# Kernel tuning notes

Hardware: AMD Instinct MI355X
Metric: run time of the kernel (lower is better)

## Reference

```python
import jax, jax.numpy as jnp
import numpy as np


def setup_inputs() -> dict:
    key = jax.random.key(0)
    k1, k2 = jax.random.split(key)
    B, S, D = 32, 1024, 384
    MAX_MEL_LEN = 8192  # >= max possible sum of durations (7*1024)
    x = jax.random.normal(k1, (B, S, D), dtype=jnp.float32)
    duration = jax.random.randint(k2, (B, S), 0, 8, dtype=jnp.int32)
    return {"x": x, "duration": duration, "max_mel_len": MAX_MEL_LEN}


def reference(x, duration, max_mel_len):
    # x: (B, S, D) float, duration: (B, S) int, max_mel_len: python int
    B, S, D = x.shape
    csum = jnp.cumsum(duration, axis=1)          # (B, S) inclusive cumsum
    mel_len = csum[:, -1]                        # (B,) expanded length per sample
    t = jnp.arange(max_mel_len, dtype=csum.dtype)  # (T,) output frame indices
    # frame t maps to token i where csum[i-1] <= t < csum[i]; side='right'
    # correctly skips zero-duration tokens (repeated csum values)
    idx = jax.vmap(lambda c: jnp.searchsorted(c, t, side='right'))(csum)  # (B, T)
    idx = jnp.clip(idx, 0, S - 1)
    out = jnp.take_along_axis(x, idx[:, :, None], axis=1)  # (B, T, D) gather
    mask = t[None, :] < mel_len[:, None]                   # (B, T) pad mask
    out = out * mask[:, :, None].astype(x.dtype)
    return out, mel_len.astype(jnp.int64)
```

## Files before the change

kernel.cpp:

```cpp
#include <hip/hip_runtime.h>


#define BATCH 32
#define SRC_S 1024
#define DIM   384
#define ROWS  32
#define C4    (DIM / 4)

typedef float f32x4 __attribute__((ext_vector_type(4)));

__global__ void lr_scan_idx_kernel(const int* __restrict__ duration,
                                   int* __restrict__ idx_g,
                                   float* __restrict__ mel_out, int T) {
    __shared__ int s[SRC_S];
    const int b = blockIdx.x;
    const int tid = threadIdx.x;
    const int d = duration[b * SRC_S + tid];
    s[tid] = d;
    for (int off = 1; off < SRC_S; off <<= 1) {
        __syncthreads();
        const int add = (tid >= off) ? s[tid - off] : 0;
        __syncthreads();
        s[tid] += add;
    }
    __syncthreads();
    const int end = s[tid];
    const int start = end - d;
    const int mel_len = s[SRC_S - 1];

    int* __restrict__ ib = idx_g + (size_t)b * T;
    for (int t = start; t < end; ++t) ib[t] = tid;
    for (int t = mel_len + tid; t < T; t += SRC_S) ib[t] = -1;

    if (tid == SRC_S - 1) mel_out[b] = (float)mel_len;
}

__global__ __launch_bounds__(256)
void lr_gather_kernel(const f32x4* __restrict__ x4,
                      const int* __restrict__ idx_g,
                      f32x4* __restrict__ out4, int T) {
    const int b = blockIdx.y;
    const int t0 = blockIdx.x * ROWS;
    const int tid = threadIdx.x;

    const int* __restrict__ ib = idx_g + (size_t)b * T + t0;
    const f32x4* __restrict__ xb = x4 + (size_t)b * SRC_S * C4;
    f32x4* __restrict__ ob = out4 + ((size_t)b * T + t0) * C4;

    #pragma unroll
    for (int k = 0; k < (ROWS * C4) / 256; ++k) {
        const int i = tid + k * 256;
        const int row = i / C4;
        const int col = i - row * C4;
        const int sidx = ib[row];
        f32x4 v = (f32x4)(0.f);
        if (sidx >= 0) v = xb[(size_t)sidx * C4 + col];
        __builtin_nontemporal_store(v, &ob[i]);
    }
}

extern "C" void kernel_launch(void* const* d_in, const int* in_sizes, int n_in,
                              void* d_out, int out_size, void* d_ws, size_t ws_size,
                              hipStream_t stream) {
    const float* x = (const float*)d_in[0];
    const int* duration = (const int*)d_in[1];
    const int T = (out_size - BATCH) / (BATCH * DIM);

    int* idx_g = (int*)d_ws;
    float* out = (float*)d_out;
    float* mel_out = out + (size_t)BATCH * T * DIM;

    lr_scan_idx_kernel<<<BATCH, SRC_S, 0, stream>>>(duration, idx_g, mel_out, T);

    dim3 grid((T + ROWS - 1) / ROWS, BATCH);
    lr_gather_kernel<<<grid, 256, 0, stream>>>((const f32x4*)x, idx_g,
                                               (f32x4*)out, T);
}
```

Before: 446.3 us.

## Use wavefront shuffle scan and XCD-aware block mapping for gather

Replaces the shared-memory Hillis-Steele scan with a two-level wavefront shuffle scan, cutting the number of block barriers. The gather grid is flattened and remapped so that all blocks of a given batch land on the same XCD, keeping that batch's source rows in one L2 slice. The mapping hardcodes 256 tiles per batch (T/ROWS) and 8 XCDs, so it only holds for T=8192 and assumes round-robin dispatch across XCDs.

```diff
diff --git a/kernel.cpp b/kernel.cpp
--- a/kernel.cpp
+++ b/kernel.cpp
@@ -6,27 +6,42 @@
 #define DIM   384
 #define ROWS  32
 #define C4    (DIM / 4)
+#define NXCD  8
 
 typedef float f32x4 __attribute__((ext_vector_type(4)));
 
 __global__ void lr_scan_idx_kernel(const int* __restrict__ duration,
                                    int* __restrict__ idx_g,
                                    float* __restrict__ mel_out, int T) {
-    __shared__ int s[SRC_S];
+    __shared__ int wsum[16];
     const int b = blockIdx.x;
     const int tid = threadIdx.x;
+    const int lane = tid & 63;
+    const int wid = tid >> 6;
     const int d = duration[b * SRC_S + tid];
-    s[tid] = d;
-    for (int off = 1; off < SRC_S; off <<= 1) {
-        __syncthreads();
-        const int add = (tid >= off) ? s[tid - off] : 0;
-        __syncthreads();
-        s[tid] += add;
+
+    int v = d;
+    #pragma unroll
+    for (int off = 1; off < 64; off <<= 1) {
+        const int n = __shfl_up(v, off, 64);
+        if (lane >= off) v += n;
+    }
+    if (lane == 63) wsum[wid] = v;
+    __syncthreads();
+    if (tid < 16) {
+        int w = wsum[tid];
+        #pragma unroll
+        for (int off = 1; off < 16; off <<= 1) {
+            const int n = __shfl_up(w, off, 64);
+            if (tid >= off) w += n;
+        }
+        wsum[tid] = w;
     }
     __syncthreads();
-    const int end = s[tid];
+    const int wbase = (wid == 0) ? 0 : wsum[wid - 1];
+    const int end = wbase + v;
     const int start = end - d;
-    const int mel_len = s[SRC_S - 1];
+    const int mel_len = wsum[15];
 
     int* __restrict__ ib = idx_g + (size_t)b * T;
     for (int t = start; t < end; ++t) ib[t] = tid;
@@ -39,8 +54,11 @@
 void lr_gather_kernel(const f32x4* __restrict__ x4,
                       const int* __restrict__ idx_g,
                       f32x4* __restrict__ out4, int T) {
-    const int b = blockIdx.y;
-    const int t0 = blockIdx.x * ROWS;
+    const int l = blockIdx.x;
+    const int xcd = l & (NXCD - 1);
+    const int j = l >> 3;
+    const int b = xcd + NXCD * (j >> 8);
+    const int t0 = (j & 255) * ROWS;
     const int tid = threadIdx.x;
 
     const int* __restrict__ ib = idx_g + (size_t)b * T + t0;
@@ -72,7 +90,7 @@
 
     lr_scan_idx_kernel<<<BATCH, SRC_S, 0, stream>>>(duration, idx_g, mel_out, T);
 
-    dim3 grid((T + ROWS - 1) / ROWS, BATCH);
-    lr_gather_kernel<<<grid, 256, 0, stream>>>((const f32x4*)x, idx_g,
-                                               (f32x4*)out, T);
+    const int nblocks = BATCH * (T / ROWS);
+    lr_gather_kernel<<<nblocks, 256, 0, stream>>>((const f32x4*)x, idx_g,
+                                                  (f32x4*)out, T);
 }
```

Measured after the change: 438.7 us. Within noise of the previous version (-1.7%).
